# Performance work log

Measured on AMD Instinct MI355X. Metric: run time of the kernel, lower is better.

## Reference

```python
import jax, jax.numpy as jnp
import numpy as np

N_NODES = 100000
N_EDGES = 600000
IN_SIZE = 128
NUM_HEADS = 8
OUT_DIM = 16  # out_size // num_heads = 128 // 8
NEG_SLOPE = 0.2


def setup_inputs() -> dict:
    key = jax.random.key(0)
    k1, k2, k3, k4, k5, k6, k7 = jax.random.split(key, 7)
    h = jax.random.normal(k1, (N_NODES, IN_SIZE), dtype=jnp.float32)
    o = jax.random.normal(k2, (N_NODES, NUM_HEADS * OUT_DIM), dtype=jnp.float32)
    # scale params for numerical sanity of exp() in edge softmax
    W = jax.random.normal(k3, (IN_SIZE, NUM_HEADS * OUT_DIM), dtype=jnp.float32) * 0.05
    attn_l = jax.random.normal(k4, (NUM_HEADS, OUT_DIM), dtype=jnp.float32) * 0.05
    attn_r = jax.random.normal(k5, (NUM_HEADS, OUT_DIM), dtype=jnp.float32) * 0.05
    src = jax.random.randint(k6, (N_EDGES,), 0, N_NODES, dtype=jnp.int64)
    dst = jax.random.randint(k7, (N_EDGES,), 0, N_NODES, dtype=jnp.int64)
    return {"h": h, "o": o, "W": W, "attn_l": attn_l, "attn_r": attn_r,
            "src": src, "dst": dst}


def reference(h, o, W, attn_l, attn_r, src, dst):
    N = h.shape[0]
    # linear projection -> per-head features [N, H, D]
    z = (h @ W).reshape(N, NUM_HEADS, OUT_DIM)
    # per-node attention logit halves [N, H]
    el = jnp.einsum('nhd,hd->nh', z, attn_l)
    er = jnp.einsum('nhd,hd->nh', z, attn_r)
    # per-edge score: message src -> dst, LeakyReLU  [E, H]
    e = jax.nn.leaky_relu(el[dst] + er[src], negative_slope=NEG_SLOPE)
    # edge softmax over incoming edges of each destination node
    m = jax.ops.segment_max(e, dst, num_segments=N)          # [N, H]
    ex = jnp.exp(e - m[dst])                                  # [E, H]
    s = jax.ops.segment_sum(ex, dst, num_segments=N)          # [N, H]
    alpha = ex / s[dst]                                       # [E, H]
    # weighted aggregate of source features  [N, H, D]
    msg = alpha[:, :, None] * z[src]                          # [E, H, D]
    agg = jax.ops.segment_sum(msg, dst, num_segments=N)
    # merge='cat' -> [N, H*D]; residual + ELU
    out = agg.reshape(N, NUM_HEADS * OUT_DIM)
    return o + jax.nn.elu(out)
```

## Files before the change

### kernel.cpp

```cpp
#include <hip/hip_runtime.h>
#include <hip/hip_bf16.h>
#include <math.h>

#define NNODES 100000
#define NEDGES 600000
#define IN 128
#define HD 128
#define NH 8
#define NEG_SLOPE 0.2f
#define RG_TOTAL (NNODES / 16)
#define NFRAG 36
#define CT_ALL 9
#define NPAD 100352
#define SCAN_BLOCKS 98
#define PACK_BLOCKS 9
#define HIST_BLOCKS ((NEDGES + 255) / 256)
#define GEMM_BLOCKS 782

typedef __attribute__((ext_vector_type(8))) short short8v;
typedef __attribute__((ext_vector_type(4))) float f32x4;

__device__ inline unsigned short f2bf(float f) {
    unsigned u = __float_as_uint(f);
    unsigned r = (u + 0x7fff + ((u >> 16) & 1)) >> 16;
    return (unsigned short)r;
}
__device__ inline float bflo(unsigned v) { return __uint_as_float(v << 16); }
__device__ inline float bfhi(unsigned v) { return __uint_as_float(v & 0xffff0000u); }

__global__ __launch_bounds__(256) void k_pack_hist(
    const float* __restrict__ W, const float* __restrict__ attn_l, const float* __restrict__ attn_r,
    short8v* __restrict__ Wb,
    const int* __restrict__ dst, int* __restrict__ cnt)
{
    const int tid = threadIdx.x;
    if (blockIdx.x < PACK_BLOCKS) {
        int slot = blockIdx.x * 256 + tid;
        int f = slot >> 6, lane = slot & 63;
        int ks = f / CT_ALL, ct = f % CT_ALL;
        int k0 = ks * 32 + (lane >> 4) * 8;
        short8v v;
        if (ct < 8) {
            int col = ct * 16 + (lane & 15);
            #pragma unroll
            for (int j = 0; j < 8; ++j) v[j] = (short)f2bf(W[(k0 + j) * HD + col]);
        } else {
            int c = lane & 15;
            const float* av = (c < 8) ? attn_l : attn_r;
            int hh = c & 7;
            #pragma unroll
            for (int j = 0; j < 8; ++j) {
                int k = k0 + j;
                float s = 0.f;
                for (int d = 0; d < 16; ++d) s += W[k * HD + hh * 16 + d] * av[hh * 16 + d];
                v[j] = (short)f2bf(s);
            }
        }
        Wb[slot] = v;
    } else {
        int e = (blockIdx.x - PACK_BLOCKS) * 256 + tid;
        if (e < NEDGES) atomicAdd(&cnt[dst[e]], 1);
    }
}

__global__ __launch_bounds__(256) void k_gemm_scan1(
    const float* __restrict__ h, const short8v* __restrict__ Wb,
    unsigned short* __restrict__ z, float* __restrict__ el, float* __restrict__ er,
    const int* __restrict__ cnt, int* __restrict__ inc, int* __restrict__ bsum)
{
    __shared__ short8v Bs[NFRAG * 64];
    __shared__ int sd[2][256];
    const int tid = threadIdx.x;

    if (blockIdx.x < SCAN_BLOCKS) {
        int gid4 = blockIdx.x * 256 + tid;
        int4 v = ((const int4*)cnt)[gid4];
        int s1 = v.x + v.y, s2 = s1 + v.z, s3 = s2 + v.w;
        sd[0][tid] = s3; __syncthreads();
        int cur = 0;
        for (int off = 1; off < 256; off <<= 1) {
            int nv = sd[cur][tid] + (tid >= off ? sd[cur][tid - off] : 0);
            sd[cur ^ 1][tid] = nv; __syncthreads();
            cur ^= 1;
        }
        int incl = sd[cur][tid];
        int eb = incl - s3;
        int4 w = make_int4(eb + v.x, eb + s1, eb + s2, eb + s3);
        ((int4*)inc)[gid4] = w;
        if (tid == 255) bsum[blockIdx.x] = incl;
        return;
    }

    {
        const float4* srcp = (const float4*)Wb;
        float4* dstp = (float4*)Bs;
        for (int i = tid; i < NFRAG * 64; i += 256) dstp[i] = srcp[i];
    }
    __syncthreads();

    const int lane  = tid & 63;
    const int rowIn = lane & 15;
    const int kgrp  = lane >> 4;
    int wid = ((blockIdx.x - SCAN_BLOCKS) * 256 + tid) >> 6;
    const int nw = GEMM_BLOCKS * 4;

    for (int rg = wid; rg < RG_TOTAL; rg += nw) {
        const int row0 = rg * 16;
        const float* hp = h + (size_t)(row0 + rowIn) * IN + kgrp * 8;

        short8v afr[4];
        #pragma unroll
        for (int ks = 0; ks < 4; ++ks) {
            float4 a0 = *(const float4*)(hp + ks * 32);
            float4 a1 = *(const float4*)(hp + ks * 32 + 4);
            short8v v;
            v[0] = (short)f2bf(a0.x); v[1] = (short)f2bf(a0.y);
            v[2] = (short)f2bf(a0.z); v[3] = (short)f2bf(a0.w);
            v[4] = (short)f2bf(a1.x); v[5] = (short)f2bf(a1.y);
            v[6] = (short)f2bf(a1.z); v[7] = (short)f2bf(a1.w);
            afr[ks] = v;
        }

        f32x4 acc[CT_ALL];
        #pragma unroll
        for (int ct = 0; ct < CT_ALL; ++ct) acc[ct] = (f32x4){0.f, 0.f, 0.f, 0.f};

        #pragma unroll
        for (int ks = 0; ks < 4; ++ks)
            #pragma unroll
            for (int ct = 0; ct < CT_ALL; ++ct)
                acc[ct] = __builtin_amdgcn_mfma_f32_16x16x32_bf16(
                    Bs[(ks * CT_ALL + ct) * 64 + lane], afr[ks], acc[ct], 0, 0, 0);

        const size_t zrow = (size_t)(row0 + rowIn) * HD;
        #pragma unroll
        for (int ct = 0; ct < 8; ++ct) {
            uint2 pk;
            pk.x = (unsigned)f2bf(acc[ct][0]) | ((unsigned)f2bf(acc[ct][1]) << 16);
            pk.y = (unsigned)f2bf(acc[ct][2]) | ((unsigned)f2bf(acc[ct][3]) << 16);
            *(uint2*)(z + zrow + ct * 16 + kgrp * 4) = pk;
        }
        {
            float4 v = make_float4(acc[8][0], acc[8][1], acc[8][2], acc[8][3]);
            int row = row0 + rowIn;
            if (kgrp < 2) *(float4*)(el + row * NH + kgrp * 4) = v;
            else          *(float4*)(er + row * NH + (kgrp - 2) * 4) = v;
        }
    }
}

__global__ __launch_bounds__(256) void kscan23(
    const int* __restrict__ cnt, const int* __restrict__ inc, const int* __restrict__ bsum,
    int* __restrict__ offs, int* __restrict__ cursor)
{
    __shared__ int bs[2][128];
    const int tid = threadIdx.x;
    if (tid < 128) bs[0][tid] = (tid < SCAN_BLOCKS) ? bsum[tid] : 0;
    __syncthreads();
    int cur = 0;
    for (int off = 1; off < 128; off <<= 1) {
        if (tid < 128) {
            int nv = bs[cur][tid] + (tid >= off ? bs[cur][tid - off] : 0);
            bs[cur ^ 1][tid] = nv;
        }
        __syncthreads();
        cur ^= 1;
    }
    const int base = (blockIdx.x == 0) ? 0 : bs[cur][blockIdx.x - 1];

    int gid4 = blockIdx.x * 256 + tid;
    int4 c = ((const int4*)cnt)[gid4];
    int4 ic = ((const int4*)inc)[gid4];
    int i0 = gid4 * 4;
    int ex[4] = { base + ic.x - c.x, base + ic.y - c.y, base + ic.z - c.z, base + ic.w - c.w };
    #pragma unroll
    for (int j = 0; j < 4; ++j) {
        int i = i0 + j;
        if (i < NNODES) { offs[i] = ex[j]; cursor[i] = ex[j]; }
        else if (i == NNODES) offs[i] = NEDGES;
    }
}

__global__ void k_scatter(const int* __restrict__ src, const int* __restrict__ dst,
                          int* __restrict__ cursor, int* __restrict__ esrc) {
    int e0 = (blockIdx.x * blockDim.x + threadIdx.x) * 4;
    if (e0 >= NEDGES) return;
    int4 s4 = *(const int4*)(src + e0);
    int4 d4 = *(const int4*)(dst + e0);
    int pos;
    pos = atomicAdd(&cursor[d4.x], 1); esrc[pos] = s4.x;
    pos = atomicAdd(&cursor[d4.y], 1); esrc[pos] = s4.y;
    pos = atomicAdd(&cursor[d4.z], 1); esrc[pos] = s4.z;
    pos = atomicAdd(&cursor[d4.w], 1); esrc[pos] = s4.w;
}

__global__ __launch_bounds__(256) void k_agg(
    const int* __restrict__ offs, const int* __restrict__ esrc,
    const float* __restrict__ el, const float* __restrict__ er,
    const unsigned short* __restrict__ z, const float* __restrict__ o,
    float* __restrict__ out)
{
    const int wid  = (blockIdx.x * blockDim.x + threadIdx.x) >> 6;
    const int lane = threadIdx.x & 63;
    if (wid >= NNODES) return;
    const int d  = wid;
    const int p0 = offs[d];
    const int n  = offs[d + 1] - p0;
    const int g  = lane & 31;
    const int e2 = lane >> 5;
    const int hh = g >> 2;
    const float el8 = el[d * NH + hh];

    const size_t obase = (size_t)d * HD + g * 4;
    const float4 ov = *(const float4*)(o + obase);

    float srun = 0.f;
    float4 acc = make_float4(0.f, 0.f, 0.f, 0.f);

    for (int c0 = 0; c0 < n; c0 += 64) {
        const int m = (n - c0 < 64) ? (n - c0) : 64;
        int sid = esrc[p0 + c0 + (lane < m ? lane : 0)];

        for (int b = 0; b < m; b += 8) {
            float erv[4]; uint2 zb[4];
            #pragma unroll
            for (int k = 0; k < 4; ++k) {
                int ei = b + k * 2 + e2;
                int eic = (ei < m) ? ei : 0;
                int s = __shfl(sid, eic, 64);
                erv[k] = er[s * NH + hh];
                zb[k]  = *(const uint2*)(z + (size_t)s * HD + g * 4);
            }
            #pragma unroll
            for (int k = 0; k < 4; ++k) {
                int ei = b + k * 2 + e2;
                float ev = el8 + erv[k];
                ev = fmaxf(ev, NEG_SLOPE * ev);
                float ex = (ei < m) ? __expf(ev) : 0.f;
                srun += ex;
                acc.x = fmaf(ex, bflo(zb[k].x), acc.x);
                acc.y = fmaf(ex, bfhi(zb[k].x), acc.y);
                acc.z = fmaf(ex, bflo(zb[k].y), acc.z);
                acc.w = fmaf(ex, bfhi(zb[k].y), acc.w);
            }
        }
    }

    srun  += __shfl_xor(srun, 32, 64);
    acc.x += __shfl_xor(acc.x, 32, 64);
    acc.y += __shfl_xor(acc.y, 32, 64);
    acc.z += __shfl_xor(acc.z, 32, 64);
    acc.w += __shfl_xor(acc.w, 32, 64);

    if (lane < 32) {
        float inv = (srun > 0.f) ? 1.f / srun : 0.f;
        float r0 = acc.x * inv, r1 = acc.y * inv, r2 = acc.z * inv, r3 = acc.w * inv;
        r0 = (r0 > 0.f) ? r0 : expm1f(r0);
        r1 = (r1 > 0.f) ? r1 : expm1f(r1);
        r2 = (r2 > 0.f) ? r2 : expm1f(r2);
        r3 = (r3 > 0.f) ? r3 : expm1f(r3);
        *(float4*)(out + obase) = make_float4(ov.x + r0, ov.y + r1, ov.z + r2, ov.w + r3);
    }
}

extern "C" void kernel_launch(void* const* d_in, const int* in_sizes, int n_in,
                              void* d_out, int out_size, void* d_ws, size_t ws_size,
                              hipStream_t stream) {
    const float* h      = (const float*)d_in[0];
    const float* o      = (const float*)d_in[1];
    const float* W      = (const float*)d_in[2];
    const float* attn_l = (const float*)d_in[3];
    const float* attn_r = (const float*)d_in[4];
    const int*   src    = (const int*)d_in[5];
    const int*   dst    = (const int*)d_in[6];
    float* out = (float*)d_out;

    char* ws = (char*)d_ws;
    unsigned short* z = (unsigned short*)(ws);
    float* el     = (float*)(ws + 25600000);
    float* er     = (float*)(ws + 28800000);
    int*   cnt    = (int*)  (ws + 32000000);
    int*   inc    = (int*)  (ws + 32401408);
    int*   offs   = (int*)  (ws + 32802816);
    int*   cursor = (int*)  (ws + 33202832);
    int*   bsum   = (int*)  (ws + 33602832);
    int*   esrc   = (int*)  (ws + 33603344);
    short8v* Wb   = (short8v*)(ws + 36003344);

    hipMemsetAsync(cnt, 0, NPAD * sizeof(int), stream);

    k_pack_hist<<<PACK_BLOCKS + HIST_BLOCKS, 256, 0, stream>>>(W, attn_l, attn_r, Wb, dst, cnt);
    k_gemm_scan1<<<SCAN_BLOCKS + GEMM_BLOCKS, 256, 0, stream>>>(h, Wb, z, el, er, cnt, inc, bsum);
    kscan23<<<SCAN_BLOCKS, 256, 0, stream>>>(cnt, inc, bsum, offs, cursor);
    k_scatter<<<(NEDGES / 4 + 255) / 256, 256, 0, stream>>>(src, dst, cursor, esrc);
    k_agg<<<(NNODES * 64 + 255) / 256, 256, 0, stream>>>(offs, esrc, el, er, z, o, out);
}
```

Baseline: 138.6 us.

## Record edge ranks in histogram pass and use hardware bf16 pack conversion

The histogram pass now keeps the return value of each atomic increment as a per-edge rank. The scatter pass then computes each edge's CSR slot as offs[dst]+rank with no second round of atomics, which also removes the cursor array. Separately, the software round-to-nearest bf16 conversions in the GEMM are replaced by the v_cvt_pk_bf16_f32 instruction, which converts two floats per instruction. In exchange, an extra rank array of 600k ints is written and read, and the histogram pass now handles four edges per thread.

```diff
diff --git a/kernel.cpp b/kernel.cpp
--- a/kernel.cpp
+++ b/kernel.cpp
@@ -14,7 +14,7 @@
 #define NPAD 100352
 #define SCAN_BLOCKS 98
 #define PACK_BLOCKS 9
-#define HIST_BLOCKS ((NEDGES + 255) / 256)
+#define HIST4_BLOCKS ((NEDGES / 4 + 255) / 256)
 #define GEMM_BLOCKS 782
 
 typedef __attribute__((ext_vector_type(8))) short short8v;
@@ -27,11 +27,16 @@
 }
 __device__ inline float bflo(unsigned v) { return __uint_as_float(v << 16); }
 __device__ inline float bfhi(unsigned v) { return __uint_as_float(v & 0xffff0000u); }
+__device__ inline unsigned cvtpk(float lo, float hi) {
+    unsigned r;
+    asm("v_cvt_pk_bf16_f32 %0, %1, %2" : "=v"(r) : "v"(lo), "v"(hi));
+    return r;
+}
 
 __global__ __launch_bounds__(256) void k_pack_hist(
     const float* __restrict__ W, const float* __restrict__ attn_l, const float* __restrict__ attn_r,
     short8v* __restrict__ Wb,
-    const int* __restrict__ dst, int* __restrict__ cnt)
+    const int* __restrict__ dst, int* __restrict__ cnt, int* __restrict__ rank)
 {
     const int tid = threadIdx.x;
     if (blockIdx.x < PACK_BLOCKS) {
@@ -58,8 +63,16 @@
         }
         Wb[slot] = v;
     } else {
-        int e = (blockIdx.x - PACK_BLOCKS) * 256 + tid;
-        if (e < NEDGES) atomicAdd(&cnt[dst[e]], 1);
+        int e0 = ((blockIdx.x - PACK_BLOCKS) * 256 + tid) * 4;
+        if (e0 < NEDGES) {
+            int4 d4 = *(const int4*)(dst + e0);
+            int4 r4;
+            r4.x = atomicAdd(&cnt[d4.x], 1);
+            r4.y = atomicAdd(&cnt[d4.y], 1);
+            r4.z = atomicAdd(&cnt[d4.z], 1);
+            r4.w = atomicAdd(&cnt[d4.w], 1);
+            *(int4*)(rank + e0) = r4;
+        }
     }
 }
 
@@ -113,12 +126,12 @@
         for (int ks = 0; ks < 4; ++ks) {
             float4 a0 = *(const float4*)(hp + ks * 32);
             float4 a1 = *(const float4*)(hp + ks * 32 + 4);
-            short8v v;
-            v[0] = (short)f2bf(a0.x); v[1] = (short)f2bf(a0.y);
-            v[2] = (short)f2bf(a0.z); v[3] = (short)f2bf(a0.w);
-            v[4] = (short)f2bf(a1.x); v[5] = (short)f2bf(a1.y);
-            v[6] = (short)f2bf(a1.z); v[7] = (short)f2bf(a1.w);
-            afr[ks] = v;
+            uint4 u;
+            u.x = cvtpk(a0.x, a0.y);
+            u.y = cvtpk(a0.z, a0.w);
+            u.z = cvtpk(a1.x, a1.y);
+            u.w = cvtpk(a1.z, a1.w);
+            afr[ks] = __builtin_bit_cast(short8v, u);
         }
 
         f32x4 acc[CT_ALL];
@@ -136,8 +149,8 @@
         #pragma unroll
         for (int ct = 0; ct < 8; ++ct) {
             uint2 pk;
-            pk.x = (unsigned)f2bf(acc[ct][0]) | ((unsigned)f2bf(acc[ct][1]) << 16);
-            pk.y = (unsigned)f2bf(acc[ct][2]) | ((unsigned)f2bf(acc[ct][3]) << 16);
+            pk.x = cvtpk(acc[ct][0], acc[ct][1]);
+            pk.y = cvtpk(acc[ct][2], acc[ct][3]);
             *(uint2*)(z + zrow + ct * 16 + kgrp * 4) = pk;
         }
         {
@@ -151,7 +164,7 @@
 
 __global__ __launch_bounds__(256) void kscan23(
     const int* __restrict__ cnt, const int* __restrict__ inc, const int* __restrict__ bsum,
-    int* __restrict__ offs, int* __restrict__ cursor)
+    int* __restrict__ offs)
 {
     __shared__ int bs[2][128];
     const int tid = threadIdx.x;
@@ -176,22 +189,23 @@
     #pragma unroll
     for (int j = 0; j < 4; ++j) {
         int i = i0 + j;
-        if (i < NNODES) { offs[i] = ex[j]; cursor[i] = ex[j]; }
+        if (i < NNODES) offs[i] = ex[j];
         else if (i == NNODES) offs[i] = NEDGES;
     }
 }
 
 __global__ void k_scatter(const int* __restrict__ src, const int* __restrict__ dst,
-                          int* __restrict__ cursor, int* __restrict__ esrc) {
+                          const int* __restrict__ rank, const int* __restrict__ offs,
+                          int* __restrict__ esrc) {
     int e0 = (blockIdx.x * blockDim.x + threadIdx.x) * 4;
     if (e0 >= NEDGES) return;
     int4 s4 = *(const int4*)(src + e0);
     int4 d4 = *(const int4*)(dst + e0);
-    int pos;
-    pos = atomicAdd(&cursor[d4.x], 1); esrc[pos] = s4.x;
-    pos = atomicAdd(&cursor[d4.y], 1); esrc[pos] = s4.y;
-    pos = atomicAdd(&cursor[d4.z], 1); esrc[pos] = s4.z;
-    pos = atomicAdd(&cursor[d4.w], 1); esrc[pos] = s4.w;
+    int4 r4 = *(const int4*)(rank + e0);
+    esrc[offs[d4.x] + r4.x] = s4.x;
+    esrc[offs[d4.y] + r4.y] = s4.y;
+    esrc[offs[d4.z] + r4.z] = s4.z;
+    esrc[offs[d4.w] + r4.w] = s4.w;
 }
 
 __global__ __launch_bounds__(256) void k_agg(
@@ -282,16 +296,16 @@
     int*   cnt    = (int*)  (ws + 32000000);
     int*   inc    = (int*)  (ws + 32401408);
     int*   offs   = (int*)  (ws + 32802816);
-    int*   cursor = (int*)  (ws + 33202832);
-    int*   bsum   = (int*)  (ws + 33602832);
-    int*   esrc   = (int*)  (ws + 33603344);
-    short8v* Wb   = (short8v*)(ws + 36003344);
+    int*   rank   = (int*)  (ws + 33202832);
+    int*   bsum   = (int*)  (ws + 35602832);
+    int*   esrc   = (int*)  (ws + 35603344);
+    short8v* Wb   = (short8v*)(ws + 38003344);
 
     hipMemsetAsync(cnt, 0, NPAD * sizeof(int), stream);
 
-    k_pack_hist<<<PACK_BLOCKS + HIST_BLOCKS, 256, 0, stream>>>(W, attn_l, attn_r, Wb, dst, cnt);
+    k_pack_hist<<<PACK_BLOCKS + HIST4_BLOCKS, 256, 0, stream>>>(W, attn_l, attn_r, Wb, dst, cnt, rank);
     k_gemm_scan1<<<SCAN_BLOCKS + GEMM_BLOCKS, 256, 0, stream>>>(h, Wb, z, el, er, cnt, inc, bsum);
-    kscan23<<<SCAN_BLOCKS, 256, 0, stream>>>(cnt, inc, bsum, offs, cursor);
-    k_scatter<<<(NEDGES / 4 + 255) / 256, 256, 0, stream>>>(src, dst, cursor, esrc);
+    kscan23<<<SCAN_BLOCKS, 256, 0, stream>>>(cnt, inc, bsum, offs);
+    k_scatter<<<(NEDGES / 4 + 255) / 256, 256, 0, stream>>>(src, dst, rank, offs, esrc);
     k_agg<<<(NNODES * 64 + 255) / 256, 256, 0, stream>>>(offs, esrc, el, er, z, o, out);
 }
```

New measurement: 117.1 us. 15.5% less time.
